# Kernel optimization log

Measured on AMD Instinct MI355X. Metric: run time of the kernel, lower is better.

## Reference

```python
import jax, jax.numpy as jnp
import numpy as np

NEG_BIG = -9e15
ALPHA = 0.2  # leakyrelu slope


def setup_inputs() -> dict:
    key = jax.random.key(0)
    k1, k2, k3, k4 = jax.random.split(key, 4)
    N, Fin, Fout = 8192, 256, 256
    input = jax.random.normal(k1, (N, Fin), dtype=jnp.float32)
    adj = jax.random.randint(k2, (N, N), 0, 2, dtype=jnp.int32)
    W = jax.random.normal(k3, (Fin, Fout), dtype=jnp.float32) * (1.0 / np.sqrt(Fin))
    a = jax.random.normal(k4, (2 * Fout, 1), dtype=jnp.float32) * (1.0 / np.sqrt(Fout))
    return {"input": input, "adj": adj, "W": W, "a": a}


def reference(input, adj, W, a):
    # h: [N, F]
    h = input @ W
    Fout = h.shape[1]
    # Fused score: e_ij = leakyrelu(h_i . a[:F] + h_j . a[F:])
    s1 = h @ a[:Fout, 0]   # [N]
    s2 = h @ a[Fout:, 0]   # [N]
    e = s1[:, None] + s2[None, :]            # [N, N]
    e = jnp.where(e >= 0, e, ALPHA * e)      # leaky relu
    e = jnp.where(adj > 0, e, NEG_BIG)       # mask
    attention = jax.nn.softmax(e, axis=1)    # row softmax
    h_prime = attention @ h                  # [N, F]
    return jax.nn.elu(h_prime)               # concat=True -> elu
```

## Files before the change

### kernel.cpp

```cpp
#include <hip/hip_runtime.h>
#include <hip/hip_bf16.h>

#define LRALPHA 0.2f
#define LOG2E 1.4426950408889634f

typedef __attribute__((ext_vector_type(8))) short frag_ab;
typedef __attribute__((ext_vector_type(4))) float frag_cd;
typedef int   iv4 __attribute__((ext_vector_type(4)));
typedef float fv4 __attribute__((ext_vector_type(4)));
typedef unsigned int uv4 __attribute__((ext_vector_type(4)));

static __device__ __forceinline__ unsigned short f2bf(float f) {
  __hip_bfloat16 b = __float2bfloat16(f);
  unsigned short u;
  __builtin_memcpy(&u, &b, 2);
  return u;
}

#if __has_builtin(__builtin_amdgcn_exp2f)
#define EXP2F(x) __builtin_amdgcn_exp2f(x)
#else
#define EXP2F(x) exp2f(x)
#endif

static __device__ __forceinline__ unsigned cvt_pk_bf16(float lo, float hi) {
  unsigned r;
  asm("v_cvt_pk_bf16_f32 %0, %1, %2" : "=v"(r) : "v"(lo), "v"(hi));
  return r;
}

static __device__ __forceinline__ void block_sync_lds() {
  __builtin_amdgcn_sched_barrier(0);
  asm volatile("s_waitcnt lgkmcnt(0)" ::: "memory");
  __builtin_amdgcn_s_barrier();
  __builtin_amdgcn_sched_barrier(0);
}

static __device__ __forceinline__ uv4 make_w(const iv4* ca, const fv4* cv,
                                             float s1r, float mr, float& zloc) {
  float w[8];
#pragma unroll
  for (int g = 0; g < 2; ++g) {
#pragma unroll
    for (int e = 0; e < 4; ++e) {
      float ee = s1r + cv[g][e];
      ee = fmaxf(ee, LRALPHA * ee);
      float ww = EXP2F(ee - mr);
      ww = ca[g][e] ? ww : 0.f;
      zloc += ww;
      w[g * 4 + e] = ww;
    }
  }
  uv4 r;
  r[0] = cvt_pk_bf16(w[0], w[1]);
  r[1] = cvt_pk_bf16(w[2], w[3]);
  r[2] = cvt_pk_bf16(w[4], w[5]);
  r[3] = cvt_pk_bf16(w[6], w[7]);
  return r;
}

__global__ __launch_bounds__(256, 4) void gat_hproj(
    const float* __restrict__ X, const float* __restrict__ W,
    const float* __restrict__ avec,
    float* __restrict__ s1, float* __restrict__ s2,
    unsigned short* __restrict__ hT) {
  const int tid = threadIdx.x;
  const int row0 = blockIdx.x * 16;
  const float* Xb = X + (size_t)row0 * 256;
  const int c = tid;

  float acc[16];
#pragma unroll
  for (int r = 0; r < 16; ++r) acc[r] = 0.f;

  for (int k = 0; k < 256; k += 4) {
    const float w0 = W[(k + 0) * 256 + c];
    const float w1 = W[(k + 1) * 256 + c];
    const float w2 = W[(k + 2) * 256 + c];
    const float w3 = W[(k + 3) * 256 + c];
#pragma unroll
    for (int r = 0; r < 16; ++r) {
      acc[r] = fmaf(Xb[r * 256 + k + 0], w0, acc[r]);
      acc[r] = fmaf(Xb[r * 256 + k + 1], w1, acc[r]);
      acc[r] = fmaf(Xb[r * 256 + k + 2], w2, acc[r]);
      acc[r] = fmaf(Xb[r * 256 + k + 3], w3, acc[r]);
    }
  }

  alignas(16) unsigned short hu[16];
#pragma unroll
  for (int r = 0; r < 16; ++r) hu[r] = f2bf(acc[r]);
  uv4* hdst = (uv4*)(hT + (size_t)c * 8192 + row0);
  hdst[0] = *(const uv4*)&hu[0];
  hdst[1] = *(const uv4*)&hu[8];

  const float a1c = avec[c];
  const float a2c = avec[256 + c];
  const int lane = tid & 63, wave = tid >> 6;
  __shared__ float r1[4][16], r2[4][16];
#pragma unroll
  for (int r = 0; r < 16; ++r) {
    float v1 = acc[r] * a1c;
    float v2 = acc[r] * a2c;
#pragma unroll
    for (int off = 32; off > 0; off >>= 1) {
      v1 += __shfl_down(v1, off);
      v2 += __shfl_down(v2, off);
    }
    if (lane == 0) { r1[wave][r] = v1; r2[wave][r] = v2; }
  }
  __syncthreads();
  if (tid < 16) {
    s1[row0 + tid] = (r1[0][tid] + r1[1][tid] + r1[2][tid] + r1[3][tid]) * LOG2E;
    s2[row0 + tid] = (r2[0][tid] + r2[1][tid] + r2[2][tid] + r2[3][tid]) * LOG2E;
  }
}

__global__ void gat_s2max(const float* __restrict__ s2, float* __restrict__ s2max) {
  const int tid = threadIdx.x;
  float m = -1e30f;
  for (int i = tid; i < 8192; i += 256) m = fmaxf(m, s2[i]);
#pragma unroll
  for (int off = 32; off > 0; off >>= 1) m = fmaxf(m, __shfl_down(m, off));
  __shared__ float ws[4];
  if ((tid & 63) == 0) ws[tid >> 6] = m;
  __syncthreads();
  if (tid == 0) s2max[0] = fmaxf(fmaxf(ws[0], ws[1]), fmaxf(ws[2], ws[3]));
}

__global__ __launch_bounds__(512, 4) void gat_attn(
    const int* __restrict__ adj, const unsigned short* __restrict__ hT,
    const float* __restrict__ s1, const float* __restrict__ s2,
    const float* __restrict__ s2maxp,
    float* __restrict__ pacc, float* __restrict__ pZ) {
  const int bid = blockIdx.x;
  const int x = bid & 7;
  const int ks = x >> 1;
  const int rb = ((bid >> 3) << 1) | (x & 1);
  const int row0 = rb * 64;
  const int jlo = ks * 2048;
  const int tid = threadIdx.x;
  const int wave = tid >> 6, lane = tid & 63;
  const int ln16 = lane & 15, quad = lane >> 4;

  __shared__ __align__(16) unsigned short P[2][64][72];
  __shared__ float Zred[64][8];

  const int r = tid >> 3, cq = tid & 7;
  const float s1r = s1[row0 + r];
  const float s2m = s2maxp[0];
  const float tmv = s1r + s2m;
  const float mr = tmv >= 0.f ? tmv : LRALPHA * tmv;

  const int* adjRow = adj + (size_t)(row0 + r) * 8192 + jlo + cq * 8;
  const float* s2p = s2 + jlo + cq * 8;

  frag_cd acc[4][2];
  const frag_cd fz = {0.f, 0.f, 0.f, 0.f};
#pragma unroll
  for (int mi = 0; mi < 4; ++mi)
#pragma unroll
    for (int ni = 0; ni < 2; ++ni) acc[mi][ni] = fz;

  float zloc = 0.f;
  const int NIT = 2048 / 64;

  {
    iv4 ca[2]; fv4 cv[2];
    ca[0] = __builtin_nontemporal_load((const iv4*)(adjRow));
    ca[1] = __builtin_nontemporal_load((const iv4*)(adjRow + 4));
    cv[0] = *(const fv4*)(s2p);
    cv[1] = *(const fv4*)(s2p + 4);
    *(uv4*)&P[0][r][cq * 8] = make_w(ca, cv, s1r, mr, zloc);
  }
  iv4 a[2]; fv4 v[2];
  a[0] = __builtin_nontemporal_load((const iv4*)(adjRow + 64));
  a[1] = __builtin_nontemporal_load((const iv4*)(adjRow + 68));
  v[0] = *(const fv4*)(s2p + 64);
  v[1] = *(const fv4*)(s2p + 68);
  block_sync_lds();

  for (int jt = 0; jt < NIT; ++jt) {
    const int cur = jt & 1, nxt = cur ^ 1;
    const size_t jbase = (size_t)(jlo + jt * 64);

    frag_ab bf[2][2];
#pragma unroll
    for (int kk = 0; kk < 2; ++kk)
#pragma unroll
      for (int ni = 0; ni < 2; ++ni) {
        const int f = wave * 32 + ni * 16 + ln16;
        bf[kk][ni] = *(const frag_ab*)(hT + (size_t)f * 8192 + jbase + kk * 32 + quad * 8);
      }

    iv4 a2[2]; fv4 v2[2];
    if (jt + 2 < NIT) {
      const int o = (jt + 2) * 64;
      a2[0] = __builtin_nontemporal_load((const iv4*)(adjRow + o));
      a2[1] = __builtin_nontemporal_load((const iv4*)(adjRow + o + 4));
      v2[0] = *(const fv4*)(s2p + o);
      v2[1] = *(const fv4*)(s2p + o + 4);
    }

    if (jt + 1 < NIT) {
      *(uv4*)&P[nxt][r][cq * 8] = make_w(a, v, s1r, mr, zloc);
    }

#pragma unroll
    for (int kk = 0; kk < 2; ++kk) {
      frag_ab af[4];
#pragma unroll
      for (int mi = 0; mi < 4; ++mi)
        af[mi] = *(const frag_ab*)&P[cur][mi * 16 + ln16][kk * 32 + quad * 8];
#pragma unroll
      for (int mi = 0; mi < 4; ++mi)
#pragma unroll
        for (int ni = 0; ni < 2; ++ni)
          acc[mi][ni] = __builtin_amdgcn_mfma_f32_16x16x32_bf16(
              af[mi], bf[kk][ni], acc[mi][ni], 0, 0, 0);
    }
    block_sync_lds();
    a[0] = a2[0]; a[1] = a2[1]; v[0] = v2[0]; v[1] = v2[1];
  }

  Zred[r][cq] = zloc;
  __syncthreads();
  if (tid < 64) {
    float z = 0.f;
#pragma unroll
    for (int q = 0; q < 8; ++q) z += Zred[tid][q];
    pZ[ks * 8192 + row0 + tid] = z;
  }

  float* paccb = pacc + ((size_t)ks * 8192 + row0) * 256;
#pragma unroll
  for (int mi = 0; mi < 4; ++mi) {
#pragma unroll
    for (int ni = 0; ni < 2; ++ni) {
      const int f = wave * 32 + ni * 16 + ln16;
#pragma unroll
      for (int reg = 0; reg < 4; ++reg) {
        const int grow = mi * 16 + quad * 4 + reg;
        __builtin_nontemporal_store(acc[mi][ni][reg], paccb + (size_t)grow * 256 + f);
      }
    }
  }
}

__global__ __launch_bounds__(256) void gat_combine(
    const float* __restrict__ pacc, const float* __restrict__ pZ,
    float* __restrict__ out) {
  const int idx = blockIdx.x * 256 + threadIdx.x;
  const int row = idx >> 6;
  const float z = pZ[row] + pZ[8192 + row] + pZ[16384 + row] + pZ[24576 + row];
  const float invz = 1.f / z;
  const size_t PSTRIDE = (size_t)8192 * 256;
  const fv4 n0 = *(const fv4*)(pacc + (size_t)idx * 4);
  const fv4 n1 = *(const fv4*)(pacc + PSTRIDE + (size_t)idx * 4);
  const fv4 n2 = *(const fv4*)(pacc + 2 * PSTRIDE + (size_t)idx * 4);
  const fv4 n3 = *(const fv4*)(pacc + 3 * PSTRIDE + (size_t)idx * 4);
  fv4 o;
#pragma unroll
  for (int e = 0; e < 4; ++e) {
    const float vsum = (n0[e] + n1[e]) + (n2[e] + n3[e]);
    const float vv = vsum * invz;
    o[e] = vv > 0.f ? vv : expm1f(vv);
  }
  *(fv4*)(out + (size_t)idx * 4) = o;
}

extern "C" void kernel_launch(void* const* d_in, const int* in_sizes, int n_in,
                              void* d_out, int out_size, void* d_ws, size_t ws_size,
                              hipStream_t stream) {
  const float* X = (const float*)d_in[0];
  const int* adj = (const int*)d_in[1];
  const float* W = (const float*)d_in[2];
  const float* avec = (const float*)d_in[3];
  float* out = (float*)d_out;

  float* wsf = (float*)d_ws;
  float* s1 = wsf;
  float* s2 = wsf + 8192;
  float* s2m = wsf + 16384;
  float* pZ = wsf + 24576;
  float* pacc = wsf + 65536;
  unsigned short* hT = (unsigned short*)(wsf + 65536 + 4 * 8192 * 256);

  hipLaunchKernelGGL(gat_hproj, dim3(512), dim3(256), 0, stream, X, W, avec, s1, s2, hT);
  hipLaunchKernelGGL(gat_s2max, dim3(1), dim3(256), 0, stream, s2, s2m);
  hipLaunchKernelGGL(gat_attn, dim3(512), dim3(512), 0, stream, adj, hT, s1, s2, s2m, pacc, pZ);
  hipLaunchKernelGGL(gat_combine, dim3(2048), dim3(256), 0, stream, pacc, pZ, out);
}
```

Baseline: 492.0 us.

## Fuse s2max, attention and combine into one full-row attention kernel

Drops the split-K over columns so each block handles 32 full rows, and computes the s2 max inside every block. Normalisation and ELU are applied in the epilogue, which removes the s2max and combine kernels and the 32 MB partial-accumulator round trip. In exchange the grid shrinks from 512 to 256 blocks with half the rows per block, and every block redundantly scans s2 for the max. The hT B-fragment loads are now amortised over fewer rows per block, so hT global traffic per output row doubles.

After: 557.7 us. 13.4% more time.

```diff
diff --git a/kernel.cpp b/kernel.cpp
--- a/kernel.cpp
+++ b/kernel.cpp
@@ -9,6 +9,7 @@
 typedef int   iv4 __attribute__((ext_vector_type(4)));
 typedef float fv4 __attribute__((ext_vector_type(4)));
 typedef unsigned int uv4 __attribute__((ext_vector_type(4)));
+typedef unsigned int uv2 __attribute__((ext_vector_type(2)));
 
 static __device__ __forceinline__ unsigned short f2bf(float f) {
   __hip_bfloat16 b = __float2bfloat16(f);
@@ -36,26 +37,21 @@
   __builtin_amdgcn_sched_barrier(0);
 }
 
-static __device__ __forceinline__ uv4 make_w(const iv4* ca, const fv4* cv,
-                                             float s1r, float mr, float& zloc) {
-  float w[8];
-#pragma unroll
-  for (int g = 0; g < 2; ++g) {
-#pragma unroll
-    for (int e = 0; e < 4; ++e) {
-      float ee = s1r + cv[g][e];
-      ee = fmaxf(ee, LRALPHA * ee);
-      float ww = EXP2F(ee - mr);
-      ww = ca[g][e] ? ww : 0.f;
-      zloc += ww;
-      w[g * 4 + e] = ww;
-    }
-  }
-  uv4 r;
+static __device__ __forceinline__ uv2 make_w4(iv4 ca, fv4 cv,
+                                              float s1r, float mr, float& zloc) {
+  float w[4];
+#pragma unroll
+  for (int e = 0; e < 4; ++e) {
+    float ee = s1r + cv[e];
+    ee = fmaxf(ee, LRALPHA * ee);
+    float ww = EXP2F(ee - mr);
+    ww = ca[e] ? ww : 0.f;
+    zloc += ww;
+    w[e] = ww;
+  }
+  uv2 r;
   r[0] = cvt_pk_bf16(w[0], w[1]);
   r[1] = cvt_pk_bf16(w[2], w[3]);
-  r[2] = cvt_pk_bf16(w[4], w[5]);
-  r[3] = cvt_pk_bf16(w[6], w[7]);
   return r;
 }
 
@@ -116,73 +112,62 @@
   }
 }
 
-__global__ void gat_s2max(const float* __restrict__ s2, float* __restrict__ s2max) {
-  const int tid = threadIdx.x;
-  float m = -1e30f;
-  for (int i = tid; i < 8192; i += 256) m = fmaxf(m, s2[i]);
-#pragma unroll
-  for (int off = 32; off > 0; off >>= 1) m = fmaxf(m, __shfl_down(m, off));
-  __shared__ float ws[4];
-  if ((tid & 63) == 0) ws[tid >> 6] = m;
-  __syncthreads();
-  if (tid == 0) s2max[0] = fmaxf(fmaxf(ws[0], ws[1]), fmaxf(ws[2], ws[3]));
-}
-
-__global__ __launch_bounds__(512, 4) void gat_attn(
+__global__ __launch_bounds__(512, 2) void gat_attn_full(
     const int* __restrict__ adj, const unsigned short* __restrict__ hT,
     const float* __restrict__ s1, const float* __restrict__ s2,
-    const float* __restrict__ s2maxp,
-    float* __restrict__ pacc, float* __restrict__ pZ) {
+    float* __restrict__ out) {
   const int bid = blockIdx.x;
-  const int x = bid & 7;
-  const int ks = x >> 1;
-  const int rb = ((bid >> 3) << 1) | (x & 1);
-  const int row0 = rb * 64;
-  const int jlo = ks * 2048;
+  const int row0 = bid * 32;
   const int tid = threadIdx.x;
   const int wave = tid >> 6, lane = tid & 63;
   const int ln16 = lane & 15, quad = lane >> 4;
 
-  __shared__ __align__(16) unsigned short P[2][64][72];
-  __shared__ float Zred[64][8];
-
-  const int r = tid >> 3, cq = tid & 7;
+  __shared__ __align__(16) unsigned short P[2][32][72];
+  __shared__ float Zred[32][16];
+  __shared__ float wred[8];
+  __shared__ float Zinv[32];
+
+  float m = -1e30f;
+  for (int i = tid; i < 8192; i += 512) m = fmaxf(m, s2[i]);
+#pragma unroll
+  for (int off = 32; off > 0; off >>= 1) m = fmaxf(m, __shfl_down(m, off));
+  if (lane == 0) wred[wave] = m;
+  __syncthreads();
+  float s2m = wred[0];
+#pragma unroll
+  for (int wv = 1; wv < 8; ++wv) s2m = fmaxf(s2m, wred[wv]);
+
+  const int r = tid >> 4;
+  const int cg = tid & 15;
   const float s1r = s1[row0 + r];
-  const float s2m = s2maxp[0];
   const float tmv = s1r + s2m;
   const float mr = tmv >= 0.f ? tmv : LRALPHA * tmv;
 
-  const int* adjRow = adj + (size_t)(row0 + r) * 8192 + jlo + cq * 8;
-  const float* s2p = s2 + jlo + cq * 8;
-
-  frag_cd acc[4][2];
+  const int* adjRow = adj + (size_t)(row0 + r) * 8192 + cg * 4;
+  const float* s2p = s2 + cg * 4;
+
+  frag_cd acc[2][2];
   const frag_cd fz = {0.f, 0.f, 0.f, 0.f};
 #pragma unroll
-  for (int mi = 0; mi < 4; ++mi)
+  for (int mi = 0; mi < 2; ++mi)
 #pragma unroll
     for (int ni = 0; ni < 2; ++ni) acc[mi][ni] = fz;
 
   float zloc = 0.f;
-  const int NIT = 2048 / 64;
+  const int NIT = 128;
 
   {
-    iv4 ca[2]; fv4 cv[2];
-    ca[0] = __builtin_nontemporal_load((const iv4*)(adjRow));
-    ca[1] = __builtin_nontemporal_load((const iv4*)(adjRow + 4));
-    cv[0] = *(const fv4*)(s2p);
-    cv[1] = *(const fv4*)(s2p + 4);
-    *(uv4*)&P[0][r][cq * 8] = make_w(ca, cv, s1r, mr, zloc);
-  }
-  iv4 a[2]; fv4 v[2];
-  a[0] = __builtin_nontemporal_load((const iv4*)(adjRow + 64));
-  a[1] = __builtin_nontemporal_load((const iv4*)(adjRow + 68));
-  v[0] = *(const fv4*)(s2p + 64);
-  v[1] = *(const fv4*)(s2p + 68);
+    iv4 ca = __builtin_nontemporal_load((const iv4*)adjRow);
+    fv4 cv = *(const fv4*)s2p;
+    *(uv2*)&P[0][r][cg * 4] = make_w4(ca, cv, s1r, mr, zloc);
+  }
+  iv4 a = __builtin_nontemporal_load((const iv4*)(adjRow + 64));
+  fv4 v = *(const fv4*)(s2p + 64);
   block_sync_lds();
 
   for (int jt = 0; jt < NIT; ++jt) {
     const int cur = jt & 1, nxt = cur ^ 1;
-    const size_t jbase = (size_t)(jlo + jt * 64);
+    const size_t jbase = (size_t)jt * 64;
 
     frag_ab bf[2][2];
 #pragma unroll
@@ -193,80 +178,59 @@
         bf[kk][ni] = *(const frag_ab*)(hT + (size_t)f * 8192 + jbase + kk * 32 + quad * 8);
       }
 
-    iv4 a2[2]; fv4 v2[2];
+    iv4 a2; fv4 v2;
     if (jt + 2 < NIT) {
       const int o = (jt + 2) * 64;
-      a2[0] = __builtin_nontemporal_load((const iv4*)(adjRow + o));
-      a2[1] = __builtin_nontemporal_load((const iv4*)(adjRow + o + 4));
-      v2[0] = *(const fv4*)(s2p + o);
-      v2[1] = *(const fv4*)(s2p + o + 4);
+      a2 = __builtin_nontemporal_load((const iv4*)(adjRow + o));
+      v2 = *(const fv4*)(s2p + o);
     }
 
     if (jt + 1 < NIT) {
-      *(uv4*)&P[nxt][r][cq * 8] = make_w(a, v, s1r, mr, zloc);
+      *(uv2*)&P[nxt][r][cg * 4] = make_w4(a, v, s1r, mr, zloc);
     }
 
 #pragma unroll
     for (int kk = 0; kk < 2; ++kk) {
-      frag_ab af[4];
-#pragma unroll
-      for (int mi = 0; mi < 4; ++mi)
+      frag_ab af[2];
+#pragma unroll
+      for (int mi = 0; mi < 2; ++mi)
         af[mi] = *(const frag_ab*)&P[cur][mi * 16 + ln16][kk * 32 + quad * 8];
 #pragma unroll
-      for (int mi = 0; mi < 4; ++mi)
+      for (int mi = 0; mi < 2; ++mi)
 #pragma unroll
         for (int ni = 0; ni < 2; ++ni)
           acc[mi][ni] = __builtin_amdgcn_mfma_f32_16x16x32_bf16(
               af[mi], bf[kk][ni], acc[mi][ni], 0, 0, 0);
     }
     block_sync_lds();
-    a[0] = a2[0]; a[1] = a2[1]; v[0] = v2[0]; v[1] = v2[1];
-  }
-
-  Zred[r][cq] = zloc;
-  __syncthreads();
-  if (tid < 64) {
+    a = a2; v = v2;
+  }
+
+  Zred[r][cg] = zloc;
+  __syncthreads();
+  if (tid < 32) {
     float z = 0.f;
 #pragma unroll
-    for (int q = 0; q < 8; ++q) z += Zred[tid][q];
-    pZ[ks * 8192 + row0 + tid] = z;
-  }
-
-  float* paccb = pacc + ((size_t)ks * 8192 + row0) * 256;
-#pragma unroll
-  for (int mi = 0; mi < 4; ++mi) {
+    for (int q = 0; q < 16; ++q) z += Zred[tid][q];
+    Zinv[tid] = 1.f / z;
+  }
+  __syncthreads();
+
+  float* outb = out + (size_t)row0 * 256;
+#pragma unroll
+  for (int mi = 0; mi < 2; ++mi) {
 #pragma unroll
     for (int ni = 0; ni < 2; ++ni) {
       const int f = wave * 32 + ni * 16 + ln16;
 #pragma unroll
       for (int reg = 0; reg < 4; ++reg) {
         const int grow = mi * 16 + quad * 4 + reg;
-        __builtin_nontemporal_store(acc[mi][ni][reg], paccb + (size_t)grow * 256 + f);
+        const float vv = acc[mi][ni][reg] * Zinv[grow];
+        const float o = vv > 0.f ? vv : expm1f(vv);
+        __builtin_nontemporal_store(o, outb + (size_t)grow * 256 + f);
       }
     }
   }
-}
-
-__global__ __launch_bounds__(256) void gat_combine(
-    const float* __restrict__ pacc, const float* __restrict__ pZ,
-    float* __restrict__ out) {
-  const int idx = blockIdx.x * 256 + threadIdx.x;
-  const int row = idx >> 6;
-  const float z = pZ[row] + pZ[8192 + row] + pZ[16384 + row] + pZ[24576 + row];
-  const float invz = 1.f / z;
-  const size_t PSTRIDE = (size_t)8192 * 256;
-  const fv4 n0 = *(const fv4*)(pacc + (size_t)idx * 4);
-  const fv4 n1 = *(const fv4*)(pacc + PSTRIDE + (size_t)idx * 4);
-  const fv4 n2 = *(const fv4*)(pacc + 2 * PSTRIDE + (size_t)idx * 4);
-  const fv4 n3 = *(const fv4*)(pacc + 3 * PSTRIDE + (size_t)idx * 4);
-  fv4 o;
-#pragma unroll
-  for (int e = 0; e < 4; ++e) {
-    const float vsum = (n0[e] + n1[e]) + (n2[e] + n3[e]);
-    const float vv = vsum * invz;
-    o[e] = vv > 0.f ? vv : expm1f(vv);
-  }
-  *(fv4*)(out + (size_t)idx * 4) = o;
 }
 
 extern "C" void kernel_launch(void* const* d_in, const int* in_sizes, int n_in,
@@ -281,13 +245,8 @@
   float* wsf = (float*)d_ws;
   float* s1 = wsf;
   float* s2 = wsf + 8192;
-  float* s2m = wsf + 16384;
-  float* pZ = wsf + 24576;
-  float* pacc = wsf + 65536;
-  unsigned short* hT = (unsigned short*)(wsf + 65536 + 4 * 8192 * 256);
+  unsigned short* hT = (unsigned short*)(wsf + 16384);
 
   hipLaunchKernelGGL(gat_hproj, dim3(512), dim3(256), 0, stream, X, W, avec, s1, s2, hT);
-  hipLaunchKernelGGL(gat_s2max, dim3(1), dim3(256), 0, stream, s2, s2m);
-  hipLaunchKernelGGL(gat_attn, dim3(512), dim3(512), 0, stream, adj, hT, s1, s2, s2m, pacc, pZ);
-  hipLaunchKernelGGL(gat_combine, dim3(2048), dim3(256), 0, stream, pacc, pZ, out);
-}
+  hipLaunchKernelGGL(gat_attn_full, dim3(256), dim3(512), 0, stream, adj, hT, s1, s2, out);
+}
```
